# Optimization experiments

Hardware: AMD Instinct MI355X
Metric: run time of the kernel (lower is better)

Reference implementation:

```python
import jax, jax.numpy as jnp
import numpy as np

N, E, IN, HID, H, OUT = 10000, 160000, 256, 64, 8, 16
NEG_SLOPE = 0.2  # PyG GATConv leaky_relu slope


def _layer_norm(x, g, b, eps=1e-5):
    m = x.mean(-1, keepdims=True)
    v = ((x - m) ** 2).mean(-1, keepdims=True)
    return (x - m) * jax.lax.rsqrt(v + eps) * g + b


def _gat_conv(x, src, dst, W, a_src, a_dst, bias, concat):
    # PyG GATConv: h = x @ W -> [N,H,C]; e_ij = leakyrelu(a_src.h_j + a_dst.h_i);
    # alpha = segment-softmax over incoming edges at dst; out_i = sum_j alpha_ij h_j
    n = x.shape[0]
    heads, c = a_src.shape
    h = (x @ W).reshape(n, heads, c)
    al_s = (h * a_src[None]).sum(-1)  # [N,H]
    al_d = (h * a_dst[None]).sum(-1)  # [N,H]
    e = al_s[src] + al_d[dst]         # [Etot,H]
    e = jnp.where(e > 0, e, NEG_SLOPE * e)
    m = jax.ops.segment_max(e, dst, num_segments=n)
    p = jnp.exp(e - m[dst])
    s = jax.ops.segment_sum(p, dst, num_segments=n)
    a = p / (s[dst] + 1e-16)          # [Etot,H]
    out = jax.ops.segment_sum(h[src] * a[:, :, None], dst, num_segments=n)
    out = out.reshape(n, heads * c) if concat else out.mean(axis=1)
    return out + bias


def setup_inputs() -> dict:
    key = jax.random.key(0)
    ks = jax.random.split(key, 12)
    d = {}
    d['x'] = jax.random.normal(ks[0], (N, IN), jnp.float32)
    d['edge_index'] = jax.random.randint(ks[1], (2, E), 0, N, jnp.int64)
    d['Wp'] = jax.random.normal(ks[2], (IN, HID * H), jnp.float32) * 0.05
    d['bp'] = jnp.zeros((HID * H,), jnp.float32)
    d['g0'] = jnp.ones((HID * H,), jnp.float32)
    d['b0'] = jnp.zeros((HID * H,), jnp.float32)
    d['W1'] = jax.random.normal(ks[3], (HID * H, HID * H), jnp.float32) * 0.05
    d['as1'] = jax.random.normal(ks[4], (H, HID), jnp.float32) * 0.1
    d['ad1'] = jax.random.normal(ks[5], (H, HID), jnp.float32) * 0.1
    d['b1'] = jnp.zeros((HID * H,), jnp.float32)
    d['g1'] = jnp.ones((HID * H,), jnp.float32)
    d['be1'] = jnp.zeros((HID * H,), jnp.float32)
    d['W2'] = jax.random.normal(ks[6], (HID * H, HID * H), jnp.float32) * 0.05
    d['as2'] = jax.random.normal(ks[7], (H, HID), jnp.float32) * 0.1
    d['ad2'] = jax.random.normal(ks[8], (H, HID), jnp.float32) * 0.1
    d['b2'] = jnp.zeros((HID * H,), jnp.float32)
    d['g2'] = jnp.ones((HID * H,), jnp.float32)
    d['be2'] = jnp.zeros((HID * H,), jnp.float32)
    d['W3'] = jax.random.normal(ks[9], (HID * H, OUT), jnp.float32) * 0.05
    d['as3'] = jax.random.normal(ks[10], (1, OUT), jnp.float32) * 0.1
    d['ad3'] = jax.random.normal(ks[11], (1, OUT), jnp.float32) * 0.1
    d['b3'] = jnp.zeros((OUT,), jnp.float32)
    d['g3'] = jnp.ones((OUT,), jnp.float32)
    d['be3'] = jnp.zeros((OUT,), jnp.float32)
    return d


def reference(x, edge_index, Wp, bp, g0, b0, W1, as1, ad1, b1, g1, be1,
              W2, as2, ad2, b2, g2, be2, W3, as3, ad3, b3, g3, be3):
    n = x.shape[0]
    loops = jnp.arange(n)  # PyG add_self_loops=True
    src = jnp.concatenate([edge_index[0], loops])
    dst = jnp.concatenate([edge_index[1], loops])
    x = jax.nn.elu(_layer_norm(x @ Wp + bp, g0, b0))
    # layer 1 (heads=8, concat) + residual
    r = x
    x = _gat_conv(x, src, dst, W1, as1, ad1, b1, True)
    x = jax.nn.elu(_layer_norm(x, g1, be1)) + r
    # layer 2 (heads=8, concat) + residual
    r = x
    x = _gat_conv(x, src, dst, W2, as2, ad2, b2, True)
    x = jax.nn.elu(_layer_norm(x, g2, be2)) + r
    # final layer (heads=1, mean/no-concat), no elu/residual
    x = _gat_conv(x, src, dst, W3, as3, ad3, b3, False)
    x = _layer_norm(x, g3, be3)
    return x
```

## Files before the change

kernel.cpp:

```cpp
#include <hip/hip_runtime.h>
#include <hip/hip_bf16.h>

#define NNODES 10000
#define NEDGES 160000
#define ETOT   (NEDGES + NNODES)
#define CIN    256
#define CH     512
#define NHEAD  8
#define HDIM   64
#define COUT   16
#define NEG_SLOPE 0.2f
#define NF ((size_t)NNODES * CH)

__device__ __forceinline__ float bf2f(uint u) {
    union { uint i; float f; } v; v.i = u << 16; return v.f;
}
__device__ __forceinline__ ushort f2bf(float x) {
    union { float f; uint i; } v; v.f = x;
    uint r = v.i + 0x7fff + ((v.i >> 16) & 1);
    return (ushort)(r >> 16);
}

typedef __attribute__((ext_vector_type(8))) short short8v;
typedef __attribute__((ext_vector_type(4))) float f32x4;

__global__ void count_deg_k(const int* __restrict__ ei, int* __restrict__ deg) {
    int eid = blockIdx.x * 256 + threadIdx.x;
    if (eid >= ETOT) return;
    int dst = (eid < NEDGES) ? ei[NEDGES + eid] : (eid - NEDGES);
    atomicAdd(&deg[dst], 1);
}

__global__ __launch_bounds__(512) void scan_k(const int* __restrict__ deg, int* __restrict__ startA) {
    __shared__ int partial[512];
    int t = threadIdx.x;
    const int per = (NNODES + 511) / 512;
    int base = t * per;
    int s = 0;
    for (int j = 0; j < per; ++j) { int idx = base + j; if (idx < NNODES) s += deg[idx]; }
    partial[t] = s;
    __syncthreads();
    for (int off = 1; off < 512; off <<= 1) {
        int v = (t >= off) ? partial[t - off] : 0;
        __syncthreads();
        partial[t] += v;
        __syncthreads();
    }
    int run = (t == 0) ? 0 : partial[t - 1];
    for (int j = 0; j < per; ++j) {
        int idx = base + j;
        if (idx < NNODES) { startA[idx] = run; run += deg[idx]; }
    }
}

__global__ void scatter_k(const int* __restrict__ ei, const int* __restrict__ startA,
                          int* __restrict__ cursor, int* __restrict__ csr_src) {
    int eid = blockIdx.x * 256 + threadIdx.x;
    if (eid >= ETOT) return;
    int src, dst;
    if (eid < NEDGES) { src = ei[eid]; dst = ei[NEDGES + eid]; }
    else { src = dst = eid - NEDGES; }
    int pos = startA[dst] + atomicAdd(&cursor[dst], 1);
    csr_src[pos] = src;
}

__global__ void convert_x_k(const float* __restrict__ x, ushort* __restrict__ xb) {
    int idx = blockIdx.x * 256 + threadIdx.x;
    if (idx >= NNODES * CIN / 4) return;
    float4 v = ((const float4*)x)[idx];
    ushort4 o; o.x = f2bf(v.x); o.y = f2bf(v.y); o.z = f2bf(v.z); o.w = f2bf(v.w);
    ((ushort4*)xb)[idx] = o;
}

__global__ __launch_bounds__(256) void convert_wT_k(const float* __restrict__ W, ushort* __restrict__ Wt,
                                                    int K, int N) {
    __shared__ float tile[32][33];
    int tx = threadIdx.x & 31, ty = threadIdx.x >> 5;
    int n0 = blockIdx.x * 32, k0 = blockIdx.y * 32;
#pragma unroll
    for (int r = 0; r < 32; r += 8)
        tile[ty + r][tx] = W[(size_t)(k0 + ty + r) * N + n0 + tx];
    __syncthreads();
#pragma unroll
    for (int r = 0; r < 32; r += 8)
        Wt[(size_t)(n0 + ty + r) * K + k0 + tx] = f2bf(tile[tx][ty + r]);
}

#define LDB 72
__global__ __launch_bounds__(256) void gemm_mfma(const ushort* __restrict__ A, const ushort* __restrict__ Bt,
                                                 const float* __restrict__ bias, ushort* __restrict__ C,
                                                 const float* __restrict__ a_src, const float* __restrict__ a_dst,
                                                 float* __restrict__ als, float* __restrict__ ald,
                                                 int M, int K) {
    __shared__ ushort Asl[64 * LDB];
    __shared__ ushort Bsl[64 * LDB];
    __shared__ float lals[2][64], lald[2][64];
    int t = threadIdx.x;
    int wid = t >> 6, lane = t & 63;
    int row0 = blockIdx.x * 64, col0 = blockIdx.y * 64;
    int wr = (wid >> 1) * 32, wc = (wid & 1) * 32;
    f32x4 acc[2][2] = {};
    int sRow = t >> 2;
    int sK = (t & 3) * 16;
    int lr = lane & 15;
    int kg = lane >> 4;

    for (int k0 = 0; k0 < K; k0 += 64) {
        int gr = row0 + sRow;
        uint4 av0 = {0u,0u,0u,0u}, av1 = {0u,0u,0u,0u};
        if (gr < M) {
            const ushort* ap = A + (size_t)gr * K + k0 + sK;
            av0 = *(const uint4*)ap; av1 = *(const uint4*)(ap + 8);
        }
        *(uint4*)(&Asl[sRow * LDB + sK]) = av0;
        *(uint4*)(&Asl[sRow * LDB + sK + 8]) = av1;
        const ushort* bp = Bt + (size_t)(col0 + sRow) * K + k0 + sK;
        *(uint4*)(&Bsl[sRow * LDB + sK]) = *(const uint4*)bp;
        *(uint4*)(&Bsl[sRow * LDB + sK + 8]) = *(const uint4*)(bp + 8);
        __syncthreads();
#pragma unroll
        for (int ks = 0; ks < 2; ++ks) {
            short8v a0 = *(const short8v*)&Asl[(wr + lr) * LDB + ks * 32 + kg * 8];
            short8v a1 = *(const short8v*)&Asl[(wr + 16 + lr) * LDB + ks * 32 + kg * 8];
            short8v b0 = *(const short8v*)&Bsl[(wc + lr) * LDB + ks * 32 + kg * 8];
            short8v b1 = *(const short8v*)&Bsl[(wc + 16 + lr) * LDB + ks * 32 + kg * 8];
            acc[0][0] = __builtin_amdgcn_mfma_f32_16x16x32_bf16(a0, b0, acc[0][0], 0, 0, 0);
            acc[0][1] = __builtin_amdgcn_mfma_f32_16x16x32_bf16(a0, b1, acc[0][1], 0, 0, 0);
            acc[1][0] = __builtin_amdgcn_mfma_f32_16x16x32_bf16(a1, b0, acc[1][0], 0, 0, 0);
            acc[1][1] = __builtin_amdgcn_mfma_f32_16x16x32_bf16(a1, b1, acc[1][1], 0, 0, 0);
        }
        __syncthreads();
    }
    float pals[2][4] = {}, pald[2][4] = {};
    bool doLog = (a_src != nullptr);
    int head = blockIdx.y;
#pragma unroll
    for (int i = 0; i < 2; ++i) {
#pragma unroll
        for (int j = 0; j < 2; ++j) {
            int cl = wc + j * 16 + lr;
            int c = col0 + cl;
            float bb = bias ? bias[c] : 0.f;
            float as_c = doLog ? a_src[head * HDIM + cl] : 0.f;
            float ad_c = doLog ? a_dst[head * HDIM + cl] : 0.f;
#pragma unroll
            for (int q = 0; q < 4; ++q) {
                int r = row0 + wr + i * 16 + kg * 4 + q;
                float hv = acc[i][j][q] + bb;
                if (r < M) C[(size_t)r * CH + c] = f2bf(hv);
                pals[i][q] += hv * as_c;
                pald[i][q] += hv * ad_c;
            }
        }
    }
    if (doLog) {
#pragma unroll
        for (int i = 0; i < 2; ++i)
#pragma unroll
            for (int q = 0; q < 4; ++q) {
#pragma unroll
                for (int off = 1; off < 16; off <<= 1) {
                    pals[i][q] += __shfl_xor(pals[i][q], off);
                    pald[i][q] += __shfl_xor(pald[i][q], off);
                }
            }
        if (lr == 0) {
#pragma unroll
            for (int i = 0; i < 2; ++i)
#pragma unroll
                for (int q = 0; q < 4; ++q) {
                    int r = wr + i * 16 + kg * 4 + q;
                    lals[wid & 1][r] = pals[i][q];
                    lald[wid & 1][r] = pald[i][q];
                }
        }
        __syncthreads();
        if (t < 64) {
            int r = row0 + t;
            if (r < M) {
                als[r * NHEAD + head] = lals[0][t] + lals[1][t];
                ald[r * NHEAD + head] = lald[0][t] + lald[1][t];
            }
        }
    }
}

__global__ __launch_bounds__(128) void ln_elu_k(const ushort* __restrict__ inb, const float* __restrict__ g,
                                                const float* __restrict__ b, ushort* __restrict__ outb) {
    int i = blockIdx.x, t = threadIdx.x;
    uint2 hv = ((const uint2*)(inb + (size_t)i * CH))[t];
    float a0 = bf2f(hv.x & 0xffff), a1 = bf2f(hv.x >> 16);
    float a2 = bf2f(hv.y & 0xffff), a3 = bf2f(hv.y >> 16);
    float s = a0 + a1 + a2 + a3;
    float s2 = a0 * a0 + a1 * a1 + a2 * a2 + a3 * a3;
#pragma unroll
    for (int off = 1; off < 64; off <<= 1) { s += __shfl_xor(s, off); s2 += __shfl_xor(s2, off); }
    __shared__ float sh[4];
    int wid = t >> 6, lane = t & 63;
    if (lane == 0) { sh[wid] = s; sh[2 + wid] = s2; }
    __syncthreads();
    float tot = sh[0] + sh[1], tot2 = sh[2] + sh[3];
    float mean = tot * (1.0f / CH);
    float var = tot2 * (1.0f / CH) - mean * mean;
    float rstd = rsqrtf(var + 1e-5f);
    float4 gv = ((const float4*)g)[t];
    float4 bv = ((const float4*)b)[t];
    float y0 = (a0 - mean) * rstd * gv.x + bv.x; y0 = y0 > 0.f ? y0 : __expf(y0) - 1.f;
    float y1 = (a1 - mean) * rstd * gv.y + bv.y; y1 = y1 > 0.f ? y1 : __expf(y1) - 1.f;
    float y2 = (a2 - mean) * rstd * gv.z + bv.z; y2 = y2 > 0.f ? y2 : __expf(y2) - 1.f;
    float y3 = (a3 - mean) * rstd * gv.w + bv.w; y3 = y3 > 0.f ? y3 : __expf(y3) - 1.f;
    ushort4 o; o.x = f2bf(y0); o.y = f2bf(y1); o.z = f2bf(y2); o.w = f2bf(y3);
    ((ushort4*)(outb + (size_t)i * CH))[t] = o;
}

__global__ __launch_bounds__(256) void agg_ln_k(const ushort* __restrict__ hb, const float* __restrict__ als,
                                                const float* __restrict__ ald, const int* __restrict__ startA,
                                                const int* __restrict__ deg, const int* __restrict__ csr,
                                                const float* __restrict__ bias, const float* __restrict__ gamma,
                                                const float* __restrict__ beta, const ushort* __restrict__ residb,
                                                ushort* __restrict__ outb) {
    __shared__ float mws[4][8];
    __shared__ float sws[4][8];
    __shared__ float accb[4][8][64];
    int t = threadIdx.x;
    int w = t >> 6, tl = t & 63;
    int i = blockIdx.x;
    int c0 = tl * 8, head = tl >> 3;
    int s0 = startA[i], d = deg[i];
    float aldv = ald[i * NHEAD + head];
    const int* cp = csr + s0;
    float m = -1e30f;
    for (int e = w; e < d; e += 4) {
        int src = cp[e];
        float ee = als[src * NHEAD + head] + aldv;
        ee = ee > 0.f ? ee : NEG_SLOPE * ee;
        m = fmaxf(m, ee);
    }
    if ((tl & 7) == 0) mws[w][head] = m;
    __syncthreads();
    m = fmaxf(fmaxf(mws[0][head], mws[1][head]), fmaxf(mws[2][head], mws[3][head]));
    float ssum = 0.f;
    float a0 = 0, a1 = 0, a2 = 0, a3 = 0, a4 = 0, a5 = 0, a6 = 0, a7 = 0;
    for (int e = w; e < d; e += 4) {
        int src = cp[e];
        float ee = als[src * NHEAD + head] + aldv;
        ee = ee > 0.f ? ee : NEG_SLOPE * ee;
        float p = __expf(ee - m);
        ssum += p;
        uint4 hv = *(const uint4*)(hb + (size_t)src * CH + c0);
        a0 += p * bf2f(hv.x & 0xffff); a1 += p * bf2f(hv.x >> 16);
        a2 += p * bf2f(hv.y & 0xffff); a3 += p * bf2f(hv.y >> 16);
        a4 += p * bf2f(hv.z & 0xffff); a5 += p * bf2f(hv.z >> 16);
        a6 += p * bf2f(hv.w & 0xffff); a7 += p * bf2f(hv.w >> 16);
    }
    if ((tl & 7) == 0) sws[w][head] = ssum;
    accb[w][0][tl] = a0; accb[w][1][tl] = a1; accb[w][2][tl] = a2; accb[w][3][tl] = a3;
    accb[w][4][tl] = a4; accb[w][5][tl] = a5; accb[w][6][tl] = a6; accb[w][7][tl] = a7;
    __syncthreads();
    ssum = sws[0][head] + sws[1][head] + sws[2][head] + sws[3][head];
    a0 = accb[0][0][tl] + accb[1][0][tl] + accb[2][0][tl] + accb[3][0][tl];
    a1 = accb[0][1][tl] + accb[1][1][tl] + accb[2][1][tl] + accb[3][1][tl];
    a2 = accb[0][2][tl] + accb[1][2][tl] + accb[2][2][tl] + accb[3][2][tl];
    a3 = accb[0][3][tl] + accb[1][3][tl] + accb[2][3][tl] + accb[3][3][tl];
    a4 = accb[0][4][tl] + accb[1][4][tl] + accb[2][4][tl] + accb[3][4][tl];
    a5 = accb[0][5][tl] + accb[1][5][tl] + accb[2][5][tl] + accb[3][5][tl];
    a6 = accb[0][6][tl] + accb[1][6][tl] + accb[2][6][tl] + accb[3][6][tl];
    a7 = accb[0][7][tl] + accb[1][7][tl] + accb[2][7][tl] + accb[3][7][tl];
    float inv = 1.0f / (ssum + 1e-16f);
    float4 bi0 = ((const float4*)bias)[tl * 2], bi1 = ((const float4*)bias)[tl * 2 + 1];
    a0 = a0 * inv + bi0.x; a1 = a1 * inv + bi0.y; a2 = a2 * inv + bi0.z; a3 = a3 * inv + bi0.w;
    a4 = a4 * inv + bi1.x; a5 = a5 * inv + bi1.y; a6 = a6 * inv + bi1.z; a7 = a7 * inv + bi1.w;
    float s = a0 + a1 + a2 + a3 + a4 + a5 + a6 + a7;
    float s2 = a0*a0 + a1*a1 + a2*a2 + a3*a3 + a4*a4 + a5*a5 + a6*a6 + a7*a7;
#pragma unroll
    for (int off = 1; off < 64; off <<= 1) { s += __shfl_xor(s, off); s2 += __shfl_xor(s2, off); }
    if (w != 0) return;
    float mean = s * (1.0f / CH);
    float var = s2 * (1.0f / CH) - mean * mean;
    float rstd = rsqrtf(var + 1e-5f);
    float4 gv0 = ((const float4*)gamma)[tl * 2], gv1 = ((const float4*)gamma)[tl * 2 + 1];
    float4 bv0 = ((const float4*)beta)[tl * 2],  bv1 = ((const float4*)beta)[tl * 2 + 1];
    uint4 rv = ((const uint4*)(residb + (size_t)i * CH))[tl];
    float y0 = (a0 - mean) * rstd * gv0.x + bv0.x; y0 = (y0 > 0.f ? y0 : __expf(y0) - 1.f) + bf2f(rv.x & 0xffff);
    float y1 = (a1 - mean) * rstd * gv0.y + bv0.y; y1 = (y1 > 0.f ? y1 : __expf(y1) - 1.f) + bf2f(rv.x >> 16);
    float y2 = (a2 - mean) * rstd * gv0.z + bv0.z; y2 = (y2 > 0.f ? y2 : __expf(y2) - 1.f) + bf2f(rv.y & 0xffff);
    float y3 = (a3 - mean) * rstd * gv0.w + bv0.w; y3 = (y3 > 0.f ? y3 : __expf(y3) - 1.f) + bf2f(rv.y >> 16);
    float y4 = (a4 - mean) * rstd * gv1.x + bv1.x; y4 = (y4 > 0.f ? y4 : __expf(y4) - 1.f) + bf2f(rv.z & 0xffff);
    float y5 = (a5 - mean) * rstd * gv1.y + bv1.y; y5 = (y5 > 0.f ? y5 : __expf(y5) - 1.f) + bf2f(rv.z >> 16);
    float y6 = (a6 - mean) * rstd * gv1.z + bv1.z; y6 = (y6 > 0.f ? y6 : __expf(y6) - 1.f) + bf2f(rv.w & 0xffff);
    float y7 = (a7 - mean) * rstd * gv1.w + bv1.w; y7 = (y7 > 0.f ? y7 : __expf(y7) - 1.f) + bf2f(rv.w >> 16);
    uint4 o;
    o.x = (uint)f2bf(y0) | ((uint)f2bf(y1) << 16);
    o.y = (uint)f2bf(y2) | ((uint)f2bf(y3) << 16);
    o.z = (uint)f2bf(y4) | ((uint)f2bf(y5) << 16);
    o.w = (uint)f2bf(y6) | ((uint)f2bf(y7) << 16);
    ((uint4*)(outb + (size_t)i * CH))[tl] = o;
}

__global__ __launch_bounds__(256) void gemm_small_k(const ushort* __restrict__ A, const float* __restrict__ W,
                                                    float* __restrict__ C) {
    int col = threadIdx.x & 15;
    int row = blockIdx.x * 16 + (threadIdx.x >> 4);
    if (row >= NNODES) return;
    const ushort* ar = A + (size_t)row * CH;
    float acc = 0.f;
#pragma unroll 8
    for (int k = 0; k < CH; k += 2) {
        uint av = *(const uint*)(ar + k);
        acc += bf2f(av & 0xffff) * W[k * COUT + col];
        acc += bf2f(av >> 16) * W[(k + 1) * COUT + col];
    }
    C[row * COUT + col] = acc;
}

__global__ __launch_bounds__(256) void agg16f_k(const float* __restrict__ h3, const float* __restrict__ as3,
                                                const float* __restrict__ ad3, const int* __restrict__ startA,
                                                const int* __restrict__ deg, const int* __restrict__ csr,
                                                const float* __restrict__ b3, const float* __restrict__ g3,
                                                const float* __restrict__ be3, float* __restrict__ out) {
    int t = threadIdx.x;
    int i = blockIdx.x * 16 + (t >> 4);
    int c = t & 15;
    if (i >= NNODES) return;
    float asc = as3[c], adc = ad3[c];
    float ald_i = h3[i * COUT + c] * adc;
#pragma unroll
    for (int off = 1; off < 16; off <<= 1) ald_i += __shfl_xor(ald_i, off, 16);
    int s0 = startA[i], d = deg[i];
    float m = -1e30f;
    for (int e = 0; e < d; ++e) {
        int src = csr[s0 + e];
        float al = h3[src * COUT + c] * asc;
#pragma unroll
        for (int off = 1; off < 16; off <<= 1) al += __shfl_xor(al, off, 16);
        float ee = al + ald_i;
        ee = ee > 0.f ? ee : NEG_SLOPE * ee;
        m = fmaxf(m, ee);
    }
    float ssum = 0.f, acc = 0.f;
    for (int e = 0; e < d; ++e) {
        int src = csr[s0 + e];
        float v = h3[src * COUT + c];
        float al = v * asc;
#pragma unroll
        for (int off = 1; off < 16; off <<= 1) al += __shfl_xor(al, off, 16);
        float ee = al + ald_i;
        ee = ee > 0.f ? ee : NEG_SLOPE * ee;
        float p = __expf(ee - m);
        ssum += p;
        acc += p * v;
    }
    acc = acc / (ssum + 1e-16f) + b3[c];
    float v = acc, v2 = acc * acc;
#pragma unroll
    for (int off = 1; off < 16; off <<= 1) { v += __shfl_xor(v, off, 16); v2 += __shfl_xor(v2, off, 16); }
    float mean = v * (1.0f / COUT);
    float var = v2 * (1.0f / COUT) - mean * mean;
    out[i * COUT + c] = (acc - mean) * rsqrtf(var + 1e-5f) * g3[c] + be3[c];
}

extern "C" void kernel_launch(void* const* d_in, const int* in_sizes, int n_in,
                              void* d_out, int out_size, void* d_ws, size_t ws_size,
                              hipStream_t stream) {
    const float* x   = (const float*)d_in[0];
    const int*   ei  = (const int*)d_in[1];
    const float* Wp  = (const float*)d_in[2];
    const float* bp  = (const float*)d_in[3];
    const float* g0  = (const float*)d_in[4];
    const float* b0  = (const float*)d_in[5];
    const float* W1  = (const float*)d_in[6];
    const float* as1 = (const float*)d_in[7];
    const float* ad1 = (const float*)d_in[8];
    const float* b1  = (const float*)d_in[9];
    const float* g1  = (const float*)d_in[10];
    const float* be1 = (const float*)d_in[11];
    const float* W2  = (const float*)d_in[12];
    const float* as2 = (const float*)d_in[13];
    const float* ad2 = (const float*)d_in[14];
    const float* b2  = (const float*)d_in[15];
    const float* g2  = (const float*)d_in[16];
    const float* be2 = (const float*)d_in[17];
    const float* W3  = (const float*)d_in[18];
    const float* as3 = (const float*)d_in[19];
    const float* ad3 = (const float*)d_in[20];
    const float* b3  = (const float*)d_in[21];
    const float* g3  = (const float*)d_in[22];
    const float* be3 = (const float*)d_in[23];

    ushort* B0  = (ushort*)d_ws;
    ushort* B1  = B0 + NF;
    ushort* B2  = B1 + NF;
    ushort* xbf = B2 + NF;
    ushort* Wpt = xbf + (size_t)NNODES * CIN;
    ushort* W1t = Wpt + (size_t)CIN * CH;
    ushort* W2t = W1t + (size_t)CH * CH;
    float* als = (float*)(W2t + (size_t)CH * CH);
    float* ald = als + NNODES * NHEAD;
    float* h3  = ald + NNODES * NHEAD;
    int* deg = (int*)(h3 + (size_t)NNODES * COUT);
    int* stA = deg + NNODES;
    int* cur = stA + NNODES;
    int* csr = cur + NNODES;

    hipMemsetAsync(deg, 0, NNODES * sizeof(int), stream);
    hipMemsetAsync(cur, 0, NNODES * sizeof(int), stream);
    count_deg_k<<<(ETOT + 255) / 256, 256, 0, stream>>>(ei, deg);
    scan_k<<<1, 512, 0, stream>>>(deg, stA);
    scatter_k<<<(ETOT + 255) / 256, 256, 0, stream>>>(ei, stA, cur, csr);

    convert_x_k<<<(NNODES * CIN / 4 + 255) / 256, 256, 0, stream>>>(x, xbf);
    convert_wT_k<<<dim3(CH / 32, CIN / 32), 256, 0, stream>>>(Wp, Wpt, CIN, CH);
    convert_wT_k<<<dim3(CH / 32, CH / 32), 256, 0, stream>>>(W1, W1t, CH, CH);
    convert_wT_k<<<dim3(CH / 32, CH / 32), 256, 0, stream>>>(W2, W2t, CH, CH);

    dim3 gg((NNODES + 63) / 64, CH / 64);

    gemm_mfma<<<gg, 256, 0, stream>>>(xbf, Wpt, bp, B0, nullptr, nullptr, nullptr, nullptr, NNODES, CIN);
    ln_elu_k<<<NNODES, 128, 0, stream>>>(B0, g0, b0, B1);

    gemm_mfma<<<gg, 256, 0, stream>>>(B1, W1t, nullptr, B2, as1, ad1, als, ald, NNODES, CH);
    agg_ln_k<<<NNODES, 256, 0, stream>>>(B2, als, ald, stA, deg, csr, b1, g1, be1, B1, B0);

    gemm_mfma<<<gg, 256, 0, stream>>>(B0, W2t, nullptr, B1, as2, ad2, als, ald, NNODES, CH);
    agg_ln_k<<<NNODES, 256, 0, stream>>>(B1, als, ald, stA, deg, csr, b2, g2, be2, B0, B2);

    gemm_small_k<<<(NNODES + 15) / 16, 256, 0, stream>>>(B2, W3, h3);
    agg16f_k<<<(NNODES + 15) / 16, 256, 0, stream>>>(h3, as3, ad3, stA, deg, csr, b3, g3, be3, (float*)d_out);
}
```

Measured before the change: 343.2 us.

## Enlarge MFMA GEMM tile to 128x128 with 64x64 per-wave subtiles

The bf16 MFMA GEMM moves from 64x64 block tiles (32x32 per wave) to 128x128 block tiles (64x64 per wave, 4x4 accumulators). Each wave's 64 columns now cover exactly one head, so the attention-logit partial sums are written directly to global memory without the shared-memory cross-wave reduction. This is meant to raise data reuse per LDS load and cut global traffic. In exchange, register pressure is higher and the grid is much smaller (79x4 blocks), which may leave compute units underused.

```diff
diff --git a/kernel.cpp b/kernel.cpp
--- a/kernel.cpp
+++ b/kernel.cpp
@@ -86,63 +86,71 @@
         Wt[(size_t)(n0 + ty + r) * K + k0 + tx] = f2bf(tile[tx][ty + r]);
 }
 
-#define LDB 72
+#define LDK 72
 __global__ __launch_bounds__(256) void gemm_mfma(const ushort* __restrict__ A, const ushort* __restrict__ Bt,
                                                  const float* __restrict__ bias, ushort* __restrict__ C,
                                                  const float* __restrict__ a_src, const float* __restrict__ a_dst,
                                                  float* __restrict__ als, float* __restrict__ ald,
                                                  int M, int K) {
-    __shared__ ushort Asl[64 * LDB];
-    __shared__ ushort Bsl[64 * LDB];
-    __shared__ float lals[2][64], lald[2][64];
+    __shared__ ushort Asl[128 * LDK];
+    __shared__ ushort Bsl[128 * LDK];
     int t = threadIdx.x;
     int wid = t >> 6, lane = t & 63;
-    int row0 = blockIdx.x * 64, col0 = blockIdx.y * 64;
-    int wr = (wid >> 1) * 32, wc = (wid & 1) * 32;
-    f32x4 acc[2][2] = {};
-    int sRow = t >> 2;
-    int sK = (t & 3) * 16;
-    int lr = lane & 15;
-    int kg = lane >> 4;
+    int lr = lane & 15, kg = lane >> 4;
+    int row0 = blockIdx.x * 128, col0 = blockIdx.y * 128;
+    int wr = (wid >> 1) * 64, wc = (wid & 1) * 64;
+    f32x4 acc[4][4] = {};
+    int sRow = t >> 1;
+    int sBase = (t & 1) * 32;
+    bool aOK = (row0 + sRow) < M;
+    const ushort* Agp = A + (size_t)(row0 + sRow) * K + sBase;
+    const ushort* Bgp = Bt + (size_t)(col0 + sRow) * K + sBase;
+    ushort* AslW = &Asl[sRow * LDK + sBase];
+    ushort* BslW = &Bsl[sRow * LDK + sBase];
 
     for (int k0 = 0; k0 < K; k0 += 64) {
-        int gr = row0 + sRow;
-        uint4 av0 = {0u,0u,0u,0u}, av1 = {0u,0u,0u,0u};
-        if (gr < M) {
-            const ushort* ap = A + (size_t)gr * K + k0 + sK;
-            av0 = *(const uint4*)ap; av1 = *(const uint4*)(ap + 8);
+        uint4 a0 = {0u,0u,0u,0u}, a1 = a0, a2 = a0, a3 = a0;
+        if (aOK) {
+            const ushort* ap = Agp + k0;
+            a0 = *(const uint4*)ap;        a1 = *(const uint4*)(ap + 8);
+            a2 = *(const uint4*)(ap + 16); a3 = *(const uint4*)(ap + 24);
         }
-        *(uint4*)(&Asl[sRow * LDB + sK]) = av0;
-        *(uint4*)(&Asl[sRow * LDB + sK + 8]) = av1;
-        const ushort* bp = Bt + (size_t)(col0 + sRow) * K + k0 + sK;
-        *(uint4*)(&Bsl[sRow * LDB + sK]) = *(const uint4*)bp;
-        *(uint4*)(&Bsl[sRow * LDB + sK + 8]) = *(const uint4*)(bp + 8);
+        const ushort* bp = Bgp + k0;
+        uint4 b0 = *(const uint4*)bp,        b1 = *(const uint4*)(bp + 8);
+        uint4 b2 = *(const uint4*)(bp + 16), b3 = *(const uint4*)(bp + 24);
+        *(uint4*)(AslW)      = a0; *(uint4*)(AslW + 8)  = a1;
+        *(uint4*)(AslW + 16) = a2; *(uint4*)(AslW + 24) = a3;
+        *(uint4*)(BslW)      = b0; *(uint4*)(BslW + 8)  = b1;
+        *(uint4*)(BslW + 16) = b2; *(uint4*)(BslW + 24) = b3;
         __syncthreads();
 #pragma unroll
         for (int ks = 0; ks < 2; ++ks) {
-            short8v a0 = *(const short8v*)&Asl[(wr + lr) * LDB + ks * 32 + kg * 8];
-            short8v a1 = *(const short8v*)&Asl[(wr + 16 + lr) * LDB + ks * 32 + kg * 8];
-            short8v b0 = *(const short8v*)&Bsl[(wc + lr) * LDB + ks * 32 + kg * 8];
-            short8v b1 = *(const short8v*)&Bsl[(wc + 16 + lr) * LDB + ks * 32 + kg * 8];
-            acc[0][0] = __builtin_amdgcn_mfma_f32_16x16x32_bf16(a0, b0, acc[0][0], 0, 0, 0);
-            acc[0][1] = __builtin_amdgcn_mfma_f32_16x16x32_bf16(a0, b1, acc[0][1], 0, 0, 0);
-            acc[1][0] = __builtin_amdgcn_mfma_f32_16x16x32_bf16(a1, b0, acc[1][0], 0, 0, 0);
-            acc[1][1] = __builtin_amdgcn_mfma_f32_16x16x32_bf16(a1, b1, acc[1][1], 0, 0, 0);
+            short8v af[4], bfr[4];
+#pragma unroll
+            for (int i = 0; i < 4; ++i) {
+                af[i]  = *(const short8v*)&Asl[(wr + i * 16 + lr) * LDK + ks * 32 + kg * 8];
+                bfr[i] = *(const short8v*)&Bsl[(wc + i * 16 + lr) * LDK + ks * 32 + kg * 8];
+            }
+#pragma unroll
+            for (int i = 0; i < 4; ++i)
+#pragma unroll
+                for (int j = 0; j < 4; ++j)
+                    acc[i][j] = __builtin_amdgcn_mfma_f32_16x16x32_bf16(af[i], bfr[j], acc[i][j], 0, 0, 0);
         }
         __syncthreads();
     }
-    float pals[2][4] = {}, pald[2][4] = {};
     bool doLog = (a_src != nullptr);
-    int head = blockIdx.y;
-#pragma unroll
-    for (int i = 0; i < 2; ++i) {
-#pragma unroll
-        for (int j = 0; j < 2; ++j) {
-            int cl = wc + j * 16 + lr;
-            int c = col0 + cl;
-            float bb = bias ? bias[c] : 0.f;
-            float as_c = doLog ? a_src[head * HDIM + cl] : 0.f;
-            float ad_c = doLog ? a_dst[head * HDIM + cl] : 0.f;
+    int head = (col0 + wc) >> 6;
+    float pals[4][4] = {}, pald[4][4] = {};
+#pragma unroll
+    for (int j = 0; j < 4; ++j) {
+        int cin = j * 16 + lr;
+        int c = col0 + wc + cin;
+        float bb = bias ? bias[c] : 0.f;
+        float as_c = doLog ? a_src[head * HDIM + cin] : 0.f;
+        float ad_c = doLog ? a_dst[head * HDIM + cin] : 0.f;
+#pragma unroll
+        for (int i = 0; i < 4; ++i) {
 #pragma unroll
             for (int q = 0; q < 4; ++q) {
                 int r = row0 + wr + i * 16 + kg * 4 + q;
@@ -155,7 +163,7 @@
     }
     if (doLog) {
 #pragma unroll
-        for (int i = 0; i < 2; ++i)
+        for (int i = 0; i < 4; ++i)
 #pragma unroll
             for (int q = 0; q < 4; ++q) {
 #pragma unroll
@@ -166,21 +174,15 @@
             }
         if (lr == 0) {
 #pragma unroll
-            for (int i = 0; i < 2; ++i)
+            for (int i = 0; i < 4; ++i)
 #pragma unroll
                 for (int q = 0; q < 4; ++q) {
-                    int r = wr + i * 16 + kg * 4 + q;
-                    lals[wid & 1][r] = pals[i][q];
-                    lald[wid & 1][r] = pald[i][q];
+                    int r = row0 + wr + i * 16 + kg * 4 + q;
+                    if (r < M) {
+                        als[r * NHEAD + head] = pals[i][q];
+                        ald[r * NHEAD + head] = pald[i][q];
+                    }
                 }
-        }
-        __syncthreads();
-        if (t < 64) {
-            int r = row0 + t;
-            if (r < M) {
-                als[r * NHEAD + head] = lals[0][t] + lals[1][t];
-                ald[r * NHEAD + head] = lald[0][t] + lald[1][t];
-            }
         }
     }
 }
@@ -413,7 +415,7 @@
     convert_wT_k<<<dim3(CH / 32, CH / 32), 256, 0, stream>>>(W1, W1t, CH, CH);
     convert_wT_k<<<dim3(CH / 32, CH / 32), 256, 0, stream>>>(W2, W2t, CH, CH);
 
-    dim3 gg((NNODES + 63) / 64, CH / 64);
+    dim3 gg((NNODES + 127) / 128, CH / 128);
 
     gemm_mfma<<<gg, 256, 0, stream>>>(xbf, Wpt, bp, B0, nullptr, nullptr, nullptr, nullptr, NNODES, CIN);
     ln_elu_k<<<NNODES, 128, 0, stream>>>(B0, g0, b0, B1);
```

Result: no change. 344.6 us (+0.4%).

## Replace tiled GEMM with full-width row-block GEMM using MFMA-prepacked weights

Applied to the files above, without the earlier changes.

Weights are pre-packed into MFMA fragment order, so each wave loads its B operands straight from global memory (L2-resident), without shared-memory staging. Each block computes a 16-row by 512-column strip, which gives every wave two whole heads and lets the attention logits be written directly instead of reduced across blocks. It also merges the x and weight conversions into one launch and folds the cursor memset into the scan. The risks are less reuse of B across rows, heavier global traffic per MFMA, and the 16-row tiles assume NNODES is a multiple of 16.

```diff
diff --git a/kernel.cpp b/kernel.cpp
--- a/kernel.cpp
+++ b/kernel.cpp
@@ -31,7 +31,8 @@
     atomicAdd(&deg[dst], 1);
 }
 
-__global__ __launch_bounds__(512) void scan_k(const int* __restrict__ deg, int* __restrict__ startA) {
+__global__ __launch_bounds__(512) void scan_k(const int* __restrict__ deg, int* __restrict__ startA,
+                                              int* __restrict__ cursor) {
     __shared__ int partial[512];
     int t = threadIdx.x;
     const int per = (NNODES + 511) / 512;
@@ -49,7 +50,7 @@
     int run = (t == 0) ? 0 : partial[t - 1];
     for (int j = 0; j < per; ++j) {
         int idx = base + j;
-        if (idx < NNODES) { startA[idx] = run; run += deg[idx]; }
+        if (idx < NNODES) { startA[idx] = run; run += deg[idx]; cursor[idx] = 0; }
     }
 }
 
@@ -64,123 +65,115 @@
     csr_src[pos] = src;
 }
 
-__global__ void convert_x_k(const float* __restrict__ x, ushort* __restrict__ xb) {
-    int idx = blockIdx.x * 256 + threadIdx.x;
-    if (idx >= NNODES * CIN / 4) return;
-    float4 v = ((const float4*)x)[idx];
-    ushort4 o; o.x = f2bf(v.x); o.y = f2bf(v.y); o.z = f2bf(v.z); o.w = f2bf(v.w);
-    ((ushort4*)xb)[idx] = o;
-}
-
-__global__ __launch_bounds__(256) void convert_wT_k(const float* __restrict__ W, ushort* __restrict__ Wt,
-                                                    int K, int N) {
-    __shared__ float tile[32][33];
-    int tx = threadIdx.x & 31, ty = threadIdx.x >> 5;
-    int n0 = blockIdx.x * 32, k0 = blockIdx.y * 32;
-#pragma unroll
-    for (int r = 0; r < 32; r += 8)
-        tile[ty + r][tx] = W[(size_t)(k0 + ty + r) * N + n0 + tx];
+__global__ void prep_k(const float* __restrict__ x, ushort* __restrict__ xbf,
+                       const float* __restrict__ Wp, ushort* __restrict__ Bp0,
+                       const float* __restrict__ W1, ushort* __restrict__ Bp1,
+                       const float* __restrict__ W2, ushort* __restrict__ Bp2) {
+    int z = blockIdx.y;
+    int tid = blockIdx.x * 256 + threadIdx.x;
+    if (z == 3) {
+        if (tid >= NNODES * CIN / 4) return;
+        float4 v = ((const float4*)x)[tid];
+        ushort4 o; o.x = f2bf(v.x); o.y = f2bf(v.y); o.z = f2bf(v.z); o.w = f2bf(v.w);
+        ((ushort4*)xbf)[tid] = o;
+        return;
+    }
+    const float* W; ushort* Bp; int K;
+    if (z == 0) { W = Wp; Bp = Bp0; K = CIN; }
+    else if (z == 1) { W = W1; Bp = Bp1; K = CH; }
+    else { W = W2; Bp = Bp2; K = CH; }
+    int total = (CH / 16) * (K / 32) * 64;
+    if (tid >= total) return;
+    int lane = tid & 63;
+    int lr = lane & 15, kg = lane >> 4;
+    int rest = tid >> 6;
+    int ks = rest % (K / 32);
+    int nb = rest / (K / 32);
+    int col = nb * 16 + lr;
+    int kbase = ks * 32 + kg * 8;
+    ushort o[8];
+#pragma unroll
+    for (int e = 0; e < 8; ++e)
+        o[e] = f2bf(W[(size_t)(kbase + e) * CH + col]);
+    uint4 pk;
+    pk.x = (uint)o[0] | ((uint)o[1] << 16);
+    pk.y = (uint)o[2] | ((uint)o[3] << 16);
+    pk.z = (uint)o[4] | ((uint)o[5] << 16);
+    pk.w = (uint)o[6] | ((uint)o[7] << 16);
+    *(uint4*)&Bp[(size_t)tid * 8] = pk;
+}
+
+__global__ __launch_bounds__(256) void gemm_fw(const ushort* __restrict__ A, const ushort* __restrict__ Bp,
+                                               const float* __restrict__ bias, ushort* __restrict__ C,
+                                               const float* __restrict__ a_src, const float* __restrict__ a_dst,
+                                               float* __restrict__ als, float* __restrict__ ald, int K) {
+    __shared__ ushort Asl[16 * 520];
+    int t = threadIdx.x;
+    int lane = t & 63, wid = t >> 6;
+    int lr = lane & 15, kg = lane >> 4;
+    int r0 = blockIdx.x * 16;
+    int LDA = K + 8;
+    if (K == 512) {
+        for (int idx = t; idx < 1024; idx += 256) {
+            int row = idx >> 6, c8 = idx & 63;
+            *(uint4*)&Asl[row * LDA + c8 * 8] = *(const uint4*)&A[(size_t)(r0 + row) * K + c8 * 8];
+        }
+    } else {
+        for (int idx = t; idx < 512; idx += 256) {
+            int row = idx >> 5, c8 = idx & 31;
+            *(uint4*)&Asl[row * LDA + c8 * 8] = *(const uint4*)&A[(size_t)(r0 + row) * K + c8 * 8];
+        }
+    }
     __syncthreads();
-#pragma unroll
-    for (int r = 0; r < 32; r += 8)
-        Wt[(size_t)(n0 + ty + r) * K + k0 + tx] = f2bf(tile[tx][ty + r]);
-}
-
-#define LDB 72
-__global__ __launch_bounds__(256) void gemm_mfma(const ushort* __restrict__ A, const ushort* __restrict__ Bt,
-                                                 const float* __restrict__ bias, ushort* __restrict__ C,
-                                                 const float* __restrict__ a_src, const float* __restrict__ a_dst,
-                                                 float* __restrict__ als, float* __restrict__ ald,
-                                                 int M, int K) {
-    __shared__ ushort Asl[64 * LDB];
-    __shared__ ushort Bsl[64 * LDB];
-    __shared__ float lals[2][64], lald[2][64];
-    int t = threadIdx.x;
-    int wid = t >> 6, lane = t & 63;
-    int row0 = blockIdx.x * 64, col0 = blockIdx.y * 64;
-    int wr = (wid >> 1) * 32, wc = (wid & 1) * 32;
-    f32x4 acc[2][2] = {};
-    int sRow = t >> 2;
-    int sK = (t & 3) * 16;
-    int lr = lane & 15;
-    int kg = lane >> 4;
-
-    for (int k0 = 0; k0 < K; k0 += 64) {
-        int gr = row0 + sRow;
-        uint4 av0 = {0u,0u,0u,0u}, av1 = {0u,0u,0u,0u};
-        if (gr < M) {
-            const ushort* ap = A + (size_t)gr * K + k0 + sK;
-            av0 = *(const uint4*)ap; av1 = *(const uint4*)(ap + 8);
+    int NST = K / 32;
+    f32x4 acc[8] = {};
+    for (int ks = 0; ks < NST; ++ks) {
+        short8v a = *(const short8v*)&Asl[lr * LDA + ks * 32 + kg * 8];
+#pragma unroll
+        for (int j = 0; j < 8; ++j) {
+            short8v b = *(const short8v*)&Bp[(((size_t)(wid * 8 + j) * NST + ks) * 64 + lane) * 8];
+            acc[j] = __builtin_amdgcn_mfma_f32_16x16x32_bf16(a, b, acc[j], 0, 0, 0);
         }
-        *(uint4*)(&Asl[sRow * LDB + sK]) = av0;
-        *(uint4*)(&Asl[sRow * LDB + sK + 8]) = av1;
-        const ushort* bp = Bt + (size_t)(col0 + sRow) * K + k0 + sK;
-        *(uint4*)(&Bsl[sRow * LDB + sK]) = *(const uint4*)bp;
-        *(uint4*)(&Bsl[sRow * LDB + sK + 8]) = *(const uint4*)(bp + 8);
-        __syncthreads();
-#pragma unroll
-        for (int ks = 0; ks < 2; ++ks) {
-            short8v a0 = *(const short8v*)&Asl[(wr + lr) * LDB + ks * 32 + kg * 8];
-            short8v a1 = *(const short8v*)&Asl[(wr + 16 + lr) * LDB + ks * 32 + kg * 8];
-            short8v b0 = *(const short8v*)&Bsl[(wc + lr) * LDB + ks * 32 + kg * 8];
-            short8v b1 = *(const short8v*)&Bsl[(wc + 16 + lr) * LDB + ks * 32 + kg * 8];
-            acc[0][0] = __builtin_amdgcn_mfma_f32_16x16x32_bf16(a0, b0, acc[0][0], 0, 0, 0);
-            acc[0][1] = __builtin_amdgcn_mfma_f32_16x16x32_bf16(a0, b1, acc[0][1], 0, 0, 0);
-            acc[1][0] = __builtin_amdgcn_mfma_f32_16x16x32_bf16(a1, b0, acc[1][0], 0, 0, 0);
-            acc[1][1] = __builtin_amdgcn_mfma_f32_16x16x32_bf16(a1, b1, acc[1][1], 0, 0, 0);
+    }
+    bool doLog = (a_src != nullptr);
+    float pals[2][4] = {}, pald[2][4] = {};
+#pragma unroll
+    for (int j = 0; j < 8; ++j) {
+        int c = wid * 128 + j * 16 + lr;
+        int cin = c & 63;
+        int hl = j >> 2;
+        float bb = bias ? bias[c] : 0.f;
+        float as_c = doLog ? a_src[(wid * 2 + hl) * HDIM + cin] : 0.f;
+        float ad_c = doLog ? a_dst[(wid * 2 + hl) * HDIM + cin] : 0.f;
+#pragma unroll
+        for (int q = 0; q < 4; ++q) {
+            int r = r0 + kg * 4 + q;
+            float hv = acc[j][q] + bb;
+            C[(size_t)r * CH + c] = f2bf(hv);
+            pals[hl][q] += hv * as_c;
+            pald[hl][q] += hv * ad_c;
         }
-        __syncthreads();
-    }
-    float pals[2][4] = {}, pald[2][4] = {};
-    bool doLog = (a_src != nullptr);
-    int head = blockIdx.y;
-#pragma unroll
-    for (int i = 0; i < 2; ++i) {
-#pragma unroll
-        for (int j = 0; j < 2; ++j) {
-            int cl = wc + j * 16 + lr;
-            int c = col0 + cl;
-            float bb = bias ? bias[c] : 0.f;
-            float as_c = doLog ? a_src[head * HDIM + cl] : 0.f;
-            float ad_c = doLog ? a_dst[head * HDIM + cl] : 0.f;
+    }
+    if (doLog) {
+#pragma unroll
+        for (int hl = 0; hl < 2; ++hl)
 #pragma unroll
             for (int q = 0; q < 4; ++q) {
-                int r = row0 + wr + i * 16 + kg * 4 + q;
-                float hv = acc[i][j][q] + bb;
-                if (r < M) C[(size_t)r * CH + c] = f2bf(hv);
-                pals[i][q] += hv * as_c;
-                pald[i][q] += hv * ad_c;
-            }
-        }
-    }
-    if (doLog) {
-#pragma unroll
-        for (int i = 0; i < 2; ++i)
-#pragma unroll
-            for (int q = 0; q < 4; ++q) {
 #pragma unroll
                 for (int off = 1; off < 16; off <<= 1) {
-                    pals[i][q] += __shfl_xor(pals[i][q], off);
-                    pald[i][q] += __shfl_xor(pald[i][q], off);
+                    pals[hl][q] += __shfl_xor(pals[hl][q], off);
+                    pald[hl][q] += __shfl_xor(pald[hl][q], off);
                 }
             }
         if (lr == 0) {
 #pragma unroll
-            for (int i = 0; i < 2; ++i)
+            for (int hl = 0; hl < 2; ++hl)
 #pragma unroll
                 for (int q = 0; q < 4; ++q) {
-                    int r = wr + i * 16 + kg * 4 + q;
-                    lals[wid & 1][r] = pals[i][q];
-                    lald[wid & 1][r] = pald[i][q];
+                    int r = r0 + kg * 4 + q;
+                    als[r * NHEAD + wid * 2 + hl] = pals[hl][q];
+                    ald[r * NHEAD + wid * 2 + hl] = pald[hl][q];
                 }
-        }
-        __syncthreads();
-        if (t < 64) {
-            int r = row0 + t;
-            if (r < M) {
-                als[r * NHEAD + head] = lals[0][t] + lals[1][t];
-                ald[r * NHEAD + head] = lald[0][t] + lald[1][t];
-            }
         }
     }
 }
@@ -391,10 +384,10 @@
     ushort* B1  = B0 + NF;
     ushort* B2  = B1 + NF;
     ushort* xbf = B2 + NF;
-    ushort* Wpt = xbf + (size_t)NNODES * CIN;
-    ushort* W1t = Wpt + (size_t)CIN * CH;
-    ushort* W2t = W1t + (size_t)CH * CH;
-    float* als = (float*)(W2t + (size_t)CH * CH);
+    ushort* Bp0 = xbf + (size_t)NNODES * CIN;
+    ushort* Bp1 = Bp0 + (size_t)CIN * CH;
+    ushort* Bp2 = Bp1 + (size_t)CH * CH;
+    float* als = (float*)(Bp2 + (size_t)CH * CH);
     float* ald = als + NNODES * NHEAD;
     float* h3  = ald + NNODES * NHEAD;
     int* deg = (int*)(h3 + (size_t)NNODES * COUT);
@@ -403,25 +396,19 @@
     int* csr = cur + NNODES;
 
     hipMemsetAsync(deg, 0, NNODES * sizeof(int), stream);
-    hipMemsetAsync(cur, 0, NNODES * sizeof(int), stream);
     count_deg_k<<<(ETOT + 255) / 256, 256, 0, stream>>>(ei, deg);
-    scan_k<<<1, 512, 0, stream>>>(deg, stA);
+    scan_k<<<1, 512, 0, stream>>>(deg, stA, cur);
     scatter_k<<<(ETOT + 255) / 256, 256, 0, stream>>>(ei, stA, cur, csr);
 
-    convert_x_k<<<(NNODES * CIN / 4 + 255) / 256, 256, 0, stream>>>(x, xbf);
-    convert_wT_k<<<dim3(CH / 32, CIN / 32), 256, 0, stream>>>(Wp, Wpt, CIN, CH);
-    convert_wT_k<<<dim3(CH / 32, CH / 32), 256, 0, stream>>>(W1, W1t, CH, CH);
-    convert_wT_k<<<dim3(CH / 32, CH / 32), 256, 0, stream>>>(W2, W2t, CH, CH);
-
-    dim3 gg((NNODES + 63) / 64, CH / 64);
-
-    gemm_mfma<<<gg, 256, 0, stream>>>(xbf, Wpt, bp, B0, nullptr, nullptr, nullptr, nullptr, NNODES, CIN);
+    prep_k<<<dim3((NNODES * CIN / 4 + 255) / 256, 4), 256, 0, stream>>>(x, xbf, Wp, Bp0, W1, Bp1, W2, Bp2);
+
+    gemm_fw<<<NNODES / 16, 256, 0, stream>>>(xbf, Bp0, bp, B0, nullptr, nullptr, nullptr, nullptr, CIN);
     ln_elu_k<<<NNODES, 128, 0, stream>>>(B0, g0, b0, B1);
 
-    gemm_mfma<<<gg, 256, 0, stream>>>(B1, W1t, nullptr, B2, as1, ad1, als, ald, NNODES, CH);
+    gemm_fw<<<NNODES / 16, 256, 0, stream>>>(B1, Bp1, nullptr, B2, as1, ad1, als, ald, CH);
     agg_ln_k<<<NNODES, 256, 0, stream>>>(B2, als, ald, stA, deg, csr, b1, g1, be1, B1, B0);
 
-    gemm_mfma<<<gg, 256, 0, stream>>>(B0, W2t, nullptr, B1, as2, ad2, als, ald, NNODES, CH);
+    gemm_fw<<<NNODES / 16, 256, 0, stream>>>(B0, Bp2, nullptr, B1, as2, ad2, als, ald, CH);
     agg_ln_k<<<NNODES, 256, 0, stream>>>(B1, als, ald, stA, deg, csr, b2, g2, be2, B0, B2);
 
     gemm_small_k<<<(NNODES + 15) / 16, 256, 0, stream>>>(B2, W3, h3);
```

Result: slower. 385.2 us (+12.2%).
